# Optimization experiments

Measured on AMD Instinct MI355X. Metric: run time of the kernel, lower is better.

The kernel has to match this reference:

```python
import jax, jax.numpy as jnp
import numpy as np

D = 1024


def setup_inputs() -> dict:
    key = jax.random.key(0)
    kx, kq, kk, kv, ko = jax.random.split(key, 5)
    scale = 0.02
    x = jax.random.normal(kx, (4, 2048, D), dtype=jnp.float32)
    Wq = jax.random.normal(kq, (D, D), dtype=jnp.float32) * scale
    Wk = jax.random.normal(kk, (D, D), dtype=jnp.float32) * scale
    Wv = jax.random.normal(kv, (D, D), dtype=jnp.float32) * scale
    Wo = jax.random.normal(ko, (D, D), dtype=jnp.float32) * scale
    return {"x": x, "Wq": Wq, "Wk": Wk, "Wv": Wv, "Wo": Wo}


def reference(x, Wq, Wk, Wv, Wo):
    # Linear projections (torch Linear: y = x @ W.T, no bias)
    q = jnp.einsum('bsd,ed->bse', x, Wq)
    k = jnp.einsum('bsd,ed->bse', x, Wk)
    v = jnp.einsum('bsd,ed->bse', x, Wv)
    d = x.shape[-1]
    # HRR binding: circular convolution of k and v along feature dim (rfft domain)
    Fk = jnp.fft.rfft(k, axis=-1)
    Fv = jnp.fft.rfft(v, axis=-1)
    Fq = jnp.fft.rfft(q, axis=-1)
    Fkv = Fk * Fv                      # bound key-value pairs, Fourier domain
    # causal cumulative memory over sequence; FFT is linear so cumsum commutes
    Fmem = jnp.cumsum(Fkv, axis=-2)    # [b, s, d//2+1] complex
    # unbind with query: circular correlation = multiply by conj(rfft(q))
    values_hat = jnp.fft.irfft(Fmem * jnp.conj(Fq), n=d, axis=-1)
    return jnp.einsum('bsd,ed->bse', values_hat, Wo)
```

## Files before the change

kernel.cpp:

```cpp
#include <hip/hip_runtime.h>
#include <hip/hip_fp16.h>

#define D_DIM 1024
#define NF 513
#define NB 4
#define NS 2048
#define NCH 128
#define CHS (NS / NCH)
#define NQKV 3072
#define KOUT 1024
#define NTOK (NB * NS)

typedef __attribute__((ext_vector_type(8))) short short8_t;
typedef __attribute__((ext_vector_type(4))) float f32x4;

__device__ inline unsigned short f2bf(float f) {
    unsigned u = __builtin_bit_cast(unsigned, f);
    u += 0x7FFFu + ((u >> 16) & 1u);
    return (unsigned short)(u >> 16);
}
__device__ inline float bf2f(unsigned short h) {
    unsigned u = ((unsigned)h) << 16;
    return __builtin_bit_cast(float, u);
}
__device__ inline unsigned pkc(float re, float im) {
    return (unsigned)f2bf(re) | ((unsigned)f2bf(im) << 16);
}
__device__ inline float2 uph(unsigned u) {
    unsigned short lo = (unsigned short)(u & 0xFFFFu), hi = (unsigned short)(u >> 16);
    return make_float2(__half2float(__builtin_bit_cast(__half, lo)),
                       __half2float(__builtin_bit_cast(__half, hi)));
}

__global__ __launch_bounds__(256) void convert_x(const float* __restrict__ src,
                                                 unsigned short* __restrict__ dst,
                                                 int n4) {
    int i = blockIdx.x * 256 + threadIdx.x;
    int stride = gridDim.x * 256;
    for (; i < n4; i += stride) {
        float4 v = reinterpret_cast<const float4*>(src)[i];
        ushort4 o;
        o.x = f2bf(v.x); o.y = f2bf(v.y); o.z = f2bf(v.z); o.w = f2bf(v.w);
        reinterpret_cast<ushort4*>(dst)[i] = o;
    }
}

__global__ __launch_bounds__(256) void transpose_w(const float* __restrict__ Wq,
                                                   const float* __restrict__ Wk,
                                                   const float* __restrict__ Wv,
                                                   float* __restrict__ WT) {
    __shared__ float tile[64][65];
    const int w = blockIdx.z;
    const float* W = (w == 0) ? Wq : (w == 1) ? Wk : Wv;
    float* T = WT + (size_t)w * 1024 * 1024;
    const int bx = blockIdx.x * 64;
    const int by = blockIdx.y * 64;
    const int tc = threadIdx.x & 63;
    const int tr = threadIdx.x >> 6;
    for (int r = tr; r < 64; r += 4)
        tile[r][tc] = W[(size_t)(by + r) * 1024 + bx + tc];
    __syncthreads();
    for (int r = tr; r < 64; r += 4)
        T[(size_t)(bx + r) * 1024 + by + tc] = tile[tc][r];
}

__device__ inline void gload_lds16(const void* g, void* l) {
    __builtin_amdgcn_global_load_lds(
        (const __attribute__((address_space(1))) void*)g,
        (__attribute__((address_space(3))) void*)l,
        16, 0, 0);
}

template <typename OutT, bool F16OUT>
__global__ __launch_bounds__(256) void gemm_bf16_bk64(const unsigned short* __restrict__ A,
                                                      const unsigned short* __restrict__ B,
                                                      OutT* __restrict__ C,
                                                      int M, int N, int K) {
    __shared__ __attribute__((aligned(16))) unsigned short ldsA[2 * 128 * 64];
    __shared__ __attribute__((aligned(16))) unsigned short ldsB[2 * 128 * 64];
    const int tid  = threadIdx.x;
    const int wave = tid >> 6;
    const int lane = tid & 63;
    const int l15  = lane & 15;
    const int q4   = (lane >> 4) & 3;
    const int h7   = l15 & 7;
    const int p0   = ((q4)     ^ h7) << 3;
    const int p1   = ((4 + q4) ^ h7) << 3;
    const int wm   = (wave >> 1) * 64;
    const int wn   = (wave & 1) * 64;
    const int bm   = blockIdx.x * 128;
    const int bn   = blockIdx.y * 128;
    const int NT   = K >> 6;

    const unsigned short* Asrc = A + (size_t)(bm + (tid >> 3)) * K + (((tid & 7) ^ ((tid >> 3) & 7)) << 3);
    const unsigned short* Bsrc = B + (size_t)(bn + (tid >> 3)) * K + (((tid & 7) ^ ((tid >> 3) & 7)) << 3);
    const size_t cstep = (size_t)32 * K;

    f32x4 acc[4][4];
#pragma unroll
    for (int i = 0; i < 4; ++i)
#pragma unroll
        for (int j = 0; j < 4; ++j)
            acc[i][j] = (f32x4){0.f, 0.f, 0.f, 0.f};

    auto STAGE = [&](int t, int b) {
        const int k0 = t << 6;
        unsigned short* la = &ldsA[b * 8192 + tid * 8];
        unsigned short* lb = &ldsB[b * 8192 + tid * 8];
        gload_lds16(Asrc + k0,             la);
        gload_lds16(Asrc + cstep + k0,     la + 2048);
        gload_lds16(Asrc + 2 * cstep + k0, la + 4096);
        gload_lds16(Asrc + 3 * cstep + k0, la + 6144);
        gload_lds16(Bsrc + k0,             lb);
        gload_lds16(Bsrc + cstep + k0,     lb + 2048);
        gload_lds16(Bsrc + 2 * cstep + k0, lb + 4096);
        gload_lds16(Bsrc + 3 * cstep + k0, lb + 6144);
    };

    STAGE(0, 0);

    for (int j = 0; j < NT; ++j) {
        const int buf = j & 1;
        if (j + 1 < NT) {
            STAGE(j + 1, buf ^ 1);
            asm volatile("s_waitcnt vmcnt(8)" ::: "memory");
        } else {
            asm volatile("s_waitcnt vmcnt(0)" ::: "memory");
        }
        __builtin_amdgcn_s_barrier();
        asm volatile("" ::: "memory");

        const unsigned short* la = &ldsA[buf * 8192];
        const unsigned short* lb = &ldsB[buf * 8192];
        {
            short8_t af[4], bfv[4];
#pragma unroll
            for (int mi = 0; mi < 4; ++mi)
                af[mi] = *reinterpret_cast<const short8_t*>(&la[(wm + mi * 16 + l15) * 64 + p0]);
#pragma unroll
            for (int ni = 0; ni < 4; ++ni)
                bfv[ni] = *reinterpret_cast<const short8_t*>(&lb[(wn + ni * 16 + l15) * 64 + p0]);
            __builtin_amdgcn_s_setprio(1);
#pragma unroll
            for (int mi = 0; mi < 4; ++mi)
#pragma unroll
                for (int ni = 0; ni < 4; ++ni)
                    acc[mi][ni] = __builtin_amdgcn_mfma_f32_16x16x32_bf16(af[mi], bfv[ni], acc[mi][ni], 0, 0, 0);
            __builtin_amdgcn_s_setprio(0);
        }
        {
            short8_t af[4], bfv[4];
#pragma unroll
            for (int mi = 0; mi < 4; ++mi)
                af[mi] = *reinterpret_cast<const short8_t*>(&la[(wm + mi * 16 + l15) * 64 + p1]);
#pragma unroll
            for (int ni = 0; ni < 4; ++ni)
                bfv[ni] = *reinterpret_cast<const short8_t*>(&lb[(wn + ni * 16 + l15) * 64 + p1]);
            __builtin_amdgcn_s_setprio(1);
#pragma unroll
            for (int mi = 0; mi < 4; ++mi)
#pragma unroll
                for (int ni = 0; ni < 4; ++ni)
                    acc[mi][ni] = __builtin_amdgcn_mfma_f32_16x16x32_bf16(af[mi], bfv[ni], acc[mi][ni], 0, 0, 0);
            __builtin_amdgcn_s_setprio(0);
        }
        __builtin_amdgcn_s_barrier();
        asm volatile("" ::: "memory");
    }

#pragma unroll
    for (int mi = 0; mi < 4; ++mi) {
        int rbase = bm + wm + mi * 16 + (lane >> 4) * 4;
#pragma unroll
        for (int ni = 0; ni < 4; ++ni) {
            int col = bn + wn + ni * 16 + l15;
#pragma unroll
            for (int j = 0; j < 4; ++j) {
                float v = acc[mi][ni][j];
                if constexpr (sizeof(OutT) == 4)
                    C[(size_t)(rbase + j) * N + col] = v;
                else if constexpr (F16OUT)
                    C[(size_t)(rbase + j) * N + col] =
                        __builtin_bit_cast(unsigned short, __float2half(v));
                else
                    C[(size_t)(rbase + j) * N + col] = f2bf(v);
            }
        }
    }
}

__device__ inline int sw(int i) { return i ^ ((i >> 4) & 15); }

__device__ inline int dr4(int n) {
    return ((n & 3) << 8) | (((n >> 2) & 3) << 6) | (((n >> 4) & 3) << 4) |
           (((n >> 6) & 3) << 2) | ((n >> 8) & 3);
}

__device__ inline float2 cmul(float2 a, float2 b) {
    return make_float2(a.x * b.x - a.y * b.y, a.x * b.y + a.y * b.x);
}

__device__ inline void fft1024_r4(float2* X, const float2* tw, int t) {
#pragma unroll
    for (int s = 0; s < 5; ++s) {
        const int L = 1 << (2 * s);
        const int r = t & (L - 1);
        const int base = ((t >> (2 * s)) << (2 * s + 2)) + r;
        float2 A  = X[sw(base)];
        float2 Bv = X[sw(base + L)];
        float2 Cv = X[sw(base + 2 * L)];
        float2 Dv = X[sw(base + 3 * L)];
        if (s != 0) {
            const int step = 1024 >> (2 * s + 2);
            Bv = cmul(Bv, tw[sw(r * step)]);
            Cv = cmul(Cv, tw[sw(2 * r * step)]);
            Dv = cmul(Dv, tw[sw(3 * r * step)]);
        }
        float2 e0 = make_float2(A.x + Cv.x, A.y + Cv.y);
        float2 e1 = make_float2(A.x - Cv.x, A.y - Cv.y);
        float2 o0 = make_float2(Bv.x + Dv.x, Bv.y + Dv.y);
        float2 o1 = make_float2(Bv.x - Dv.x, Bv.y - Dv.y);
        X[sw(base)]         = make_float2(e0.x + o0.x, e0.y + o0.y);
        X[sw(base + L)]     = make_float2(e1.x + o1.y, e1.y - o1.x);
        X[sw(base + 2 * L)] = make_float2(e0.x - o0.x, e0.y - o0.y);
        X[sw(base + 3 * L)] = make_float2(e1.x - o1.y, e1.y + o1.x);
        __syncthreads();
    }
}

__device__ inline void twiddle_local(float2* twL, int tid) {
    for (int k = tid; k < 768; k += 256) {
        float ang = -6.283185307179586f * (float)k / 1024.0f;
        float s, c;
        sincosf(ang, &s, &c);
        twL[sw(k)] = make_float2(c, s);
    }
}

__global__ __launch_bounds__(256) void wf_all(const float* __restrict__ WT,
                                              const float* __restrict__ Wo,
                                              unsigned short* __restrict__ WF,
                                              unsigned short* __restrict__ Wt) {
    __shared__ __attribute__((aligned(16))) float2 X[1024];
    __shared__ __attribute__((aligned(16))) float2 twL[768];
    const int tid = threadIdx.x;
    const int y = blockIdx.y;
    const int i0 = blockIdx.x * 2;
    twiddle_local(twL, tid);
    const float* r0 = (y < 3) ? (WT + (size_t)y * 1048576 + (size_t)i0 * 1024)
                              : (Wo + (size_t)i0 * 1024);
    const float* r1 = r0 + 1024;
    for (int n = tid; n < 1024; n += 256)
        X[sw(dr4(n))] = make_float2(r0[n], r1[n]);
    __syncthreads();
    fft1024_r4(X, twL, tid);
    if (y < 3) {
        const int rbase = y * 1024;
        for (int f = tid; f < NF; f += 256) {
            float2 Zj = X[sw(f)];
            float2 Zm = X[sw((1024 - f) & 1023)];
            float re0 = 0.5f * (Zj.x + Zm.x), im0 = 0.5f * (Zj.y - Zm.y);
            float re1 = 0.5f * (Zj.y + Zm.y), im1 = 0.5f * (Zm.x - Zj.x);
            if (f == 0) {
                WF[(size_t)(rbase + 0) * 1024 + i0]     = f2bf(re0);
                WF[(size_t)(rbase + 0) * 1024 + i0 + 1] = f2bf(re1);
            } else if (f == 512) {
                WF[(size_t)(rbase + 1) * 1024 + i0]     = f2bf(re0);
                WF[(size_t)(rbase + 1) * 1024 + i0 + 1] = f2bf(re1);
            } else {
                WF[(size_t)(rbase + 2 * f)     * 1024 + i0]     = f2bf(re0);
                WF[(size_t)(rbase + 2 * f + 1) * 1024 + i0]     = f2bf(im0);
                WF[(size_t)(rbase + 2 * f)     * 1024 + i0 + 1] = f2bf(re1);
                WF[(size_t)(rbase + 2 * f + 1) * 1024 + i0 + 1] = f2bf(im1);
            }
        }
    } else {
        unsigned short* o0 = Wt + (size_t)i0 * KOUT;
        unsigned short* o1 = o0 + KOUT;
        const float inv = 1.0f / 1024.0f;
        for (int f = tid; f < NF; f += 256) {
            float2 Zj = X[sw(f)];
            float2 Zm = X[sw((1024 - f) & 1023)];
            float re0 = 0.5f * (Zj.x + Zm.x), im0 = 0.5f * (Zj.y - Zm.y);
            float re1 = 0.5f * (Zj.y + Zm.y), im1 = 0.5f * (Zm.x - Zj.x);
            if (f == 0) {
                o0[0] = f2bf(re0 * inv);
                o1[0] = f2bf(re1 * inv);
            } else if (f == 512) {
                o0[1] = f2bf(re0 * inv);
                o1[1] = f2bf(re1 * inv);
            } else {
                float c = 2.0f * inv;
                o0[2 * f]     = f2bf(re0 * c);
                o0[2 * f + 1] = f2bf(im0 * c);
                o1[2 * f]     = f2bf(re1 * c);
                o1[2 * f + 1] = f2bf(im1 * c);
            }
        }
    }
}

__global__ __launch_bounds__(256) void hrr_chunk_sum(const unsigned* __restrict__ F,
                                                     float2* __restrict__ part) {
    int f = blockIdx.x * 256 + threadIdx.x;
    int ch = blockIdx.y, b = blockIdx.z;
    size_t base = ((size_t)b * NS + (size_t)ch * CHS) * 1536;
    float2* pp = part + (size_t)(b * NCH + ch) * NF;
    if (f == 0) {
        float s0 = 0.f, s512 = 0.f;
        for (int i = 0; i < CHS; ++i) {
            size_t row = base + (size_t)i * 1536;
            float2 k = uph(F[row + 512]);
            float2 v = uph(F[row + 1024]);
            s0   += k.x * v.x;
            s512 += k.y * v.y;
        }
        pp[0]   = make_float2(s0, 0.f);
        pp[512] = make_float2(s512, 0.f);
    } else {
        float sx = 0.f, sy = 0.f;
        for (int i = 0; i < CHS; ++i) {
            size_t row = base + (size_t)i * 1536;
            float2 k = uph(F[row + 512 + f]);
            float2 v = uph(F[row + 1024 + f]);
            sx += k.x * v.x - k.y * v.y;
            sy += k.x * v.y + k.y * v.x;
        }
        pp[f] = make_float2(sx, sy);
    }
}

__global__ __launch_bounds__(256) void hrr_prefix(float2* __restrict__ part) {
    int f = blockIdx.x * 256 + threadIdx.x;
    int b = blockIdx.y;
    if (f >= NF) return;
    float rx = 0.f, ry = 0.f;
    for (int ch = 0; ch < NCH; ++ch) {
        size_t idx = ((size_t)b * NCH + ch) * NF + f;
        float2 t = part[idx];
        part[idx] = make_float2(rx, ry);
        rx += t.x; ry += t.y;
    }
}

__global__ __launch_bounds__(256) void hrr_scan_apply(const unsigned* __restrict__ F,
                                                      const float2* __restrict__ part,
                                                      unsigned* __restrict__ U) {
    int f = blockIdx.x * 256 + threadIdx.x;
    int ch = blockIdx.y, b = blockIdx.z;
    size_t base  = ((size_t)b * NS + (size_t)ch * CHS) * 1536;
    size_t ubase = ((size_t)b * NS + (size_t)ch * CHS) * 512;
    const float2* pp = part + (size_t)(b * NCH + ch) * NF;
    if (f == 0) {
        float r0 = pp[0].x, r512 = pp[512].x;
        for (int i = 0; i < CHS; ++i) {
            size_t row = base + (size_t)i * 1536;
            float2 k = uph(F[row + 512]);
            float2 v = uph(F[row + 1024]);
            float2 q = uph(F[row]);
            r0   += k.x * v.x;
            r512 += k.y * v.y;
            U[ubase + (size_t)i * 512] = pkc(r0 * q.x, r512 * q.y);
        }
    } else {
        float2 p = pp[f];
        float rx = p.x, ry = p.y;
        for (int i = 0; i < CHS; ++i) {
            size_t row = base + (size_t)i * 1536;
            float2 k = uph(F[row + 512 + f]);
            float2 v = uph(F[row + 1024 + f]);
            rx += k.x * v.x - k.y * v.y;
            ry += k.x * v.y + k.y * v.x;
            float2 q = uph(F[row + f]);
            U[ubase + (size_t)i * 512 + f] = pkc(rx * q.x + ry * q.y,
                                                 ry * q.x - rx * q.y);
        }
    }
}

extern "C" void kernel_launch(void* const* d_in, const int* in_sizes, int n_in,
                              void* d_out, int out_size, void* d_ws, size_t ws_size,
                              hipStream_t stream) {
    const float* x  = (const float*)d_in[0];
    const float* Wq = (const float*)d_in[1];
    const float* Wk = (const float*)d_in[2];
    const float* Wv = (const float*)d_in[3];
    const float* Wo = (const float*)d_in[4];
    float* out = (float*)d_out;

    char* ws = (char*)d_ws;
    unsigned short* F_all = (unsigned short*)(ws + 0);
    unsigned short* U     = (unsigned short*)(ws + 50331648);
    float2*         part  = (float2*)        (ws + 67108864);
    unsigned short* WF    = (unsigned short*)(ws + 69210112);
    unsigned short* Wt    = (unsigned short*)(ws + 75501568);
    unsigned short* xb    = (unsigned short*)(ws + 77598720);
    float* WT = (float*)U;

    convert_x<<<2048, 256, 0, stream>>>(x, xb, NTOK * D_DIM / 4);

    transpose_w<<<dim3(16, 16, 3), 256, 0, stream>>>(Wq, Wk, Wv, WT);
    wf_all<<<dim3(512, 4), 256, 0, stream>>>(WT, Wo, WF, Wt);

    dim3 gq(NTOK / 128, NQKV / 128);
    gemm_bf16_bk64<unsigned short, true><<<gq, 256, 0, stream>>>(xb, WF, F_all, NTOK, NQKV, D_DIM);

    dim3 gs(2, NCH, NB);
    hrr_chunk_sum<<<gs, 256, 0, stream>>>((const unsigned*)F_all, part);
    hrr_prefix<<<dim3(3, NB), 256, 0, stream>>>(part);
    hrr_scan_apply<<<gs, 256, 0, stream>>>((const unsigned*)F_all, part, (unsigned*)U);

    dim3 go(NTOK / 128, D_DIM / 128);
    gemm_bf16_bk64<float, false><<<go, 256, 0, stream>>>(U, Wt, out, NTOK, D_DIM, KOUT);
}
```

Before: 156.2 us.

## Merge x conversion and weight transpose into one kernel; double scan chunk count

Fuses the bf16 conversion of x and the transpose of Wq/Wk/Wv into a single launch by splitting the grid by block id, which removes one kernel launch and lets the two independent jobs run side by side. It also raises the number of sequence chunks in the HRR scan from 128 to 256, so the chunk-sum and apply kernels get more parallel blocks with shorter serial chains, at the cost of a larger partial-sum buffer and a longer prefix pass. The workspace offsets are moved to make room for the larger partials buffer.

```diff
diff --git a/kernel.cpp b/kernel.cpp
--- a/kernel.cpp
+++ b/kernel.cpp
@@ -5,7 +5,7 @@
 #define NF 513
 #define NB 4
 #define NS 2048
-#define NCH 128
+#define NCH 256
 #define CHS (NS / NCH)
 #define NQKV 3072
 #define KOUT 1024
@@ -32,36 +32,39 @@
                        __half2float(__builtin_bit_cast(__half, hi)));
 }
 
-__global__ __launch_bounds__(256) void convert_x(const float* __restrict__ src,
-                                                 unsigned short* __restrict__ dst,
-                                                 int n4) {
-    int i = blockIdx.x * 256 + threadIdx.x;
-    int stride = gridDim.x * 256;
-    for (; i < n4; i += stride) {
-        float4 v = reinterpret_cast<const float4*>(src)[i];
-        ushort4 o;
-        o.x = f2bf(v.x); o.y = f2bf(v.y); o.z = f2bf(v.z); o.w = f2bf(v.w);
-        reinterpret_cast<ushort4*>(dst)[i] = o;
-    }
-}
-
-__global__ __launch_bounds__(256) void transpose_w(const float* __restrict__ Wq,
-                                                   const float* __restrict__ Wk,
-                                                   const float* __restrict__ Wv,
-                                                   float* __restrict__ WT) {
-    __shared__ float tile[64][65];
-    const int w = blockIdx.z;
-    const float* W = (w == 0) ? Wq : (w == 1) ? Wk : Wv;
-    float* T = WT + (size_t)w * 1024 * 1024;
-    const int bx = blockIdx.x * 64;
-    const int by = blockIdx.y * 64;
-    const int tc = threadIdx.x & 63;
-    const int tr = threadIdx.x >> 6;
-    for (int r = tr; r < 64; r += 4)
-        tile[r][tc] = W[(size_t)(by + r) * 1024 + bx + tc];
-    __syncthreads();
-    for (int r = tr; r < 64; r += 4)
-        T[(size_t)(bx + r) * 1024 + by + tc] = tile[tc][r];
+__global__ __launch_bounds__(256) void prep(const float* __restrict__ x,
+                                            const float* __restrict__ Wq,
+                                            const float* __restrict__ Wk,
+                                            const float* __restrict__ Wv,
+                                            unsigned short* __restrict__ xb,
+                                            float* __restrict__ WT) {
+    const int bid = blockIdx.x;
+    if (bid < 2048) {
+        const int n4 = NTOK * D_DIM / 4;
+        int i = bid * 256 + threadIdx.x;
+        for (; i < n4; i += 2048 * 256) {
+            float4 v = reinterpret_cast<const float4*>(x)[i];
+            ushort4 o;
+            o.x = f2bf(v.x); o.y = f2bf(v.y); o.z = f2bf(v.z); o.w = f2bf(v.w);
+            reinterpret_cast<ushort4*>(xb)[i] = o;
+        }
+    } else {
+        __shared__ float tile[64][65];
+        const int t = bid - 2048;
+        const int w = t >> 8;
+        const int ti = t & 255;
+        const float* W = (w == 0) ? Wq : (w == 1) ? Wk : Wv;
+        float* T = WT + (size_t)w * 1024 * 1024;
+        const int bx = (ti & 15) * 64;
+        const int by = (ti >> 4) * 64;
+        const int tc = threadIdx.x & 63;
+        const int tr = threadIdx.x >> 6;
+        for (int r = tr; r < 64; r += 4)
+            tile[r][tc] = W[(size_t)(by + r) * 1024 + bx + tc];
+        __syncthreads();
+        for (int r = tr; r < 64; r += 4)
+            T[(size_t)(bx + r) * 1024 + by + tc] = tile[tc][r];
+    }
 }
 
 __device__ inline void gload_lds16(const void* g, void* l) {
@@ -392,14 +395,12 @@
     unsigned short* F_all = (unsigned short*)(ws + 0);
     unsigned short* U     = (unsigned short*)(ws + 50331648);
     float2*         part  = (float2*)        (ws + 67108864);
-    unsigned short* WF    = (unsigned short*)(ws + 69210112);
-    unsigned short* Wt    = (unsigned short*)(ws + 75501568);
-    unsigned short* xb    = (unsigned short*)(ws + 77598720);
+    unsigned short* WF    = (unsigned short*)(ws + 71311360);
+    unsigned short* Wt    = (unsigned short*)(ws + 77602816);
+    unsigned short* xb    = (unsigned short*)(ws + 79699968);
     float* WT = (float*)U;
 
-    convert_x<<<2048, 256, 0, stream>>>(x, xb, NTOK * D_DIM / 4);
-
-    transpose_w<<<dim3(16, 16, 3), 256, 0, stream>>>(Wq, Wk, Wv, WT);
+    prep<<<2048 + 768, 256, 0, stream>>>(x, Wq, Wk, Wv, xb, WT);
     wf_all<<<dim3(512, 4), 256, 0, stream>>>(WT, Wo, WF, Wt);
 
     dim3 gq(NTOK / 128, NQKV / 128);
```

New measurement: 162.6 us. +4.1%, slower.
